# Optimization experiments

Hardware: AMD Instinct MI355X
Metric: run time of the kernel (lower is better)

The kernel has to match this reference:

```python
import jax, jax.numpy as jnp
import numpy as np

EPS = 1e-15
MAX_ATANH = 1.0 - 1e-5
V = 2097152   # total nodes (B*N*L flattened)
E = 8388608   # edges, ~avg degree 4 (temporal + parent/child)
ATT = 16
MAXD = 512    # mixer embedding table size
# curvature c = 1.0 (registered buffer, constant)


def _mobius_add(a, b):
    # Poincare ball Mobius addition, c = 1
    a2 = jnp.sum(a * a, -1, keepdims=True)
    b2 = jnp.sum(b * b, -1, keepdims=True)
    ab = jnp.sum(a * b, -1, keepdims=True)
    num = (1.0 + 2.0 * ab + b2) * a + (1.0 - a2) * b
    den = 1.0 + 2.0 * ab + a2 * b2
    return num / jnp.maximum(den, EPS)


def _log_map_x(x, y):
    # log_x(y): tangent vector at x pointing to y (c = 1)
    sub = _mobius_add(-x, y)
    n = jnp.maximum(jnp.linalg.norm(sub, axis=-1, keepdims=True), EPS)
    lam = 2.0 / jnp.maximum(1.0 - jnp.sum(x * x, -1, keepdims=True), EPS)
    return (2.0 / lam) * jnp.arctanh(jnp.minimum(n, MAX_ATANH)) * (sub / n)


def _exp_map_x(x, v):
    # exp_x(v) (c = 1)
    n = jnp.maximum(jnp.linalg.norm(v, axis=-1, keepdims=True), EPS)
    lam = 2.0 / jnp.maximum(1.0 - jnp.sum(x * x, -1, keepdims=True), EPS)
    return _mobius_add(x, jnp.tanh(0.5 * lam * n) * (v / n))


def setup_inputs() -> dict:
    key = jax.random.key(0)
    ks = jax.random.split(key, 8)
    # node embeddings strictly inside the unit ball: exp0 of a small tangent vec
    v0 = 0.5 * jax.random.normal(ks[0], (V, 2), jnp.float32)
    n0 = jnp.maximum(jnp.linalg.norm(v0, axis=-1, keepdims=True), EPS)
    x = jnp.tanh(n0) * v0 / n0
    edge_index = jax.random.randint(ks[1], (2, E), 0, V)
    depth = jax.random.randint(ks[2], (V,), 0, MAXD)
    W1 = jax.random.normal(ks[3], (2, ATT), jnp.float32) / jnp.sqrt(2.0)
    b1 = 0.1 * jax.random.normal(ks[4], (ATT,), jnp.float32)
    W2 = jax.random.normal(ks[5], (ATT, 1), jnp.float32) / jnp.sqrt(float(ATT))
    eta = jnp.float32(1.0)
    depth_scale = 1.0 + 0.01 * jax.random.normal(ks[6], (MAXD,), jnp.float32)
    depth_theta = 0.01 * jax.random.normal(ks[7], (MAXD,), jnp.float32)
    return {"x": x, "W1": W1, "b1": b1, "W2": W2, "eta": eta,
            "depth_scale": depth_scale, "depth_theta": depth_theta,
            "edge_index": edge_index, "depth": depth}


def reference(x, W1, b1, W2, eta, depth_scale, depth_theta, edge_index, depth):
    row, col = edge_index[0], edge_index[1]
    xi = x[row]                      # [E,2] gather target endpoints
    xj = x[col]                      # [E,2] gather source endpoints
    v_ij = _log_map_x(xi, xj)        # [E,2] hyperbolic log-map
    # small per-edge MLP scorer: Linear(2,16) -> GELU(exact) -> Linear(16,1)
    h = jax.nn.gelu(v_ij @ W1 + b1, approximate=False)
    scores = (h @ W2)[:, 0]          # [E]
    # segment softmax over target node (row)
    mx = jax.ops.segment_max(scores, row, num_segments=V)
    e = jnp.exp(scores - mx[row])
    den = jax.ops.segment_sum(e, row, num_segments=V)
    alpha = e / jnp.maximum(den[row], EPS)
    # scatter-add aggregate in tangent space
    m = jax.ops.segment_sum(alpha[:, None] * v_ij, row, num_segments=V)  # [V,2]
    # depth-gated mixer: per-node scale + 2D rotation
    d = jnp.minimum(depth, MAXD - 1)
    k = depth_scale[d][:, None]
    ang = depth_theta[d]
    ca, sa = jnp.cos(ang), jnp.sin(ang)
    m = k * jnp.stack([ca * m[:, 0] - sa * m[:, 1],
                       sa * m[:, 0] + ca * m[:, 1]], axis=-1)
    # exp-map update
    return _exp_map_x(x, eta * m)
```

## Files before the change

### kernel.cpp

```cpp
#include <hip/hip_runtime.h>
#include <math.h>

#define EPSF 1e-15f
#define MAX_ATANH (1.0f - 1e-5f)
#define ATT 16

#define LOG_NPB 10
#define NPB (1 << LOG_NPB)
#define MAXB 2048
#define NBLK 512

#define TDIM 512
#define TSPAN 12.5f
#define TSTEP (TSPAN / (float)(TDIM - 1))
#define TSCALE ((float)(TDIM - 1) / TSPAN)
#define TOFF (6.25f * TSCALE)

__device__ __forceinline__ float fast_atanh(float z) {
    return 0.5f * __logf(__fdividef(1.0f + z, 1.0f - z));
}

__device__ __forceinline__ float fast_tanh(float z) {
    return 1.0f - __fdividef(2.0f, __expf(2.0f * z) + 1.0f);
}

__device__ __forceinline__ float gelu_exact(float u) {
    return 0.5f * u * (1.0f + erff(u * 0.70710678118654752f));
}

__global__ void __launch_bounds__(256) build_table_kernel(
        const float* __restrict__ W1, const float* __restrict__ b1,
        const float* __restrict__ W2, float2* __restrict__ tab) {
    const int idx = blockIdx.x * 256 + threadIdx.x;
    if (idx >= TDIM * TDIM) return;
    const int iy = idx >> 9;
    const int ix = idx & (TDIM - 1);
    const float vy  = fmaf((float)iy, TSTEP, -6.25f);
    const float vx0 = fmaf((float)ix, TSTEP, -6.25f);
    const float vx1 = fmaf((float)min(ix + 1, TDIM - 1), TSTEP, -6.25f);
    float s0 = 0.0f, s1 = 0.0f;
    #pragma unroll
    for (int k = 0; k < ATT; ++k) {
        const float w1x = W1[k], w1y = W1[ATT + k], bb = b1[k], w2 = W2[k];
        const float u0 = fmaf(vx0, w1x, fmaf(vy, w1y, bb));
        const float u1 = fmaf(vx1, w1x, fmaf(vy, w1y, bb));
        s0 = fmaf(gelu_exact(u0), w2, s0);
        s1 = fmaf(gelu_exact(u1), w2, s1);
    }
    tab[idx] = make_float2(s0, s1);
}

__global__ void __launch_bounds__(256) hist_kernel(const int* __restrict__ row,
                                                   int E, int B,
                                                   unsigned* __restrict__ counts ) {
    __shared__ unsigned h[MAXB];
    for (int i = threadIdx.x; i < B; i += 256) h[i] = 0u;
    __syncthreads();
    const int T = gridDim.x * 256;
    const int nv = E >> 2;
    const int4* row4 = (const int4*)row;
    for (int i = blockIdx.x * 256 + threadIdx.x; i < nv; i += T) {
        const int4 r = row4[i];
        atomicAdd(&h[((unsigned)r.x) >> LOG_NPB], 1u);
        atomicAdd(&h[((unsigned)r.y) >> LOG_NPB], 1u);
        atomicAdd(&h[((unsigned)r.z) >> LOG_NPB], 1u);
        atomicAdd(&h[((unsigned)r.w) >> LOG_NPB], 1u);
    }
    for (int e = (nv << 2) + blockIdx.x * 256 + threadIdx.x; e < E; e += T)
        atomicAdd(&h[((unsigned)row[e]) >> LOG_NPB], 1u);
    __syncthreads();
    for (int i = threadIdx.x; i < B; i += 256)
        counts[(size_t)i * gridDim.x + blockIdx.x] = h[i];
}

__global__ void __launch_bounds__(256) scan_blocks_kernel(const unsigned* __restrict__ counts,
                                                          unsigned* __restrict__ within,
                                                          unsigned* __restrict__ totals) {
    const int b = blockIdx.x;
    const unsigned* src = counts + (size_t)b * NBLK;
    unsigned* dst = within + (size_t)b * NBLK;
    __shared__ unsigned s[256];
    unsigned v0, v1;
    {
        const uint2 v = ((const uint2*)src)[threadIdx.x];
        v0 = v.x; v1 = v.y;
    }
    s[threadIdx.x] = v0 + v1;
    __syncthreads();
    for (int off = 1; off < 256; off <<= 1) {
        unsigned t = (threadIdx.x >= off) ? s[threadIdx.x - off] : 0u;
        __syncthreads();
        s[threadIdx.x] += t;
        __syncthreads();
    }
    unsigned base = (threadIdx.x > 0) ? s[threadIdx.x - 1] : 0u;
    uint2 o;
    o.x = base; o.y = base + v0;
    ((uint2*)dst)[threadIdx.x] = o;
    if (threadIdx.x == 255) totals[b] = s[255];
}

__global__ void __launch_bounds__(256) scan_totals_kernel(const unsigned* __restrict__ totals,
                                                          unsigned* __restrict__ base, int B) {
    __shared__ unsigned s[256];
    unsigned vals[8];
    const int i0 = threadIdx.x * 8;
    unsigned sum = 0u;
    #pragma unroll
    for (int k = 0; k < 8; ++k) {
        vals[k] = (i0 + k < B) ? totals[i0 + k] : 0u;
        sum += vals[k];
    }
    s[threadIdx.x] = sum;
    __syncthreads();
    for (int off = 1; off < 256; off <<= 1) {
        unsigned t = (threadIdx.x >= off) ? s[threadIdx.x - off] : 0u;
        __syncthreads();
        s[threadIdx.x] += t;
        __syncthreads();
    }
    unsigned b0 = (threadIdx.x > 0) ? s[threadIdx.x - 1] : 0u;
    #pragma unroll
    for (int k = 0; k < 8; ++k) {
        if (i0 + k < B) base[i0 + k] = b0;
        b0 += vals[k];
    }
    if (threadIdx.x == 255) base[B] = s[255];
}

__global__ void __launch_bounds__(256) scatter_kernel(const int* __restrict__ row,
                                                      const int* __restrict__ col,
                                                      int E, int B,
                                                      const unsigned* __restrict__ base,
                                                      const unsigned* __restrict__ within,
                                                      unsigned* __restrict__ payload) {
    __shared__ unsigned cur[MAXB];
    const int nblk = gridDim.x;
    for (int i = threadIdx.x; i < B; i += 256)
        cur[i] = base[i] + within[(size_t)i * nblk + blockIdx.x];
    __syncthreads();
    const int T = nblk * 256;
    const int nv = E >> 2;
    const int4* row4 = (const int4*)row;
    const int4* col4 = (const int4*)col;
    for (int i = blockIdx.x * 256 + threadIdx.x; i < nv; i += T) {
        const int4 r = row4[i];
        const int4 c = col4[i];
        {
            const unsigned rr = (unsigned)r.x;
            const unsigned pos = atomicAdd(&cur[rr >> LOG_NPB], 1u);
            payload[pos] = ((rr & (NPB - 1)) << 21) | (unsigned)c.x;
        }
        {
            const unsigned rr = (unsigned)r.y;
            const unsigned pos = atomicAdd(&cur[rr >> LOG_NPB], 1u);
            payload[pos] = ((rr & (NPB - 1)) << 21) | (unsigned)c.y;
        }
        {
            const unsigned rr = (unsigned)r.z;
            const unsigned pos = atomicAdd(&cur[rr >> LOG_NPB], 1u);
            payload[pos] = ((rr & (NPB - 1)) << 21) | (unsigned)c.z;
        }
        {
            const unsigned rr = (unsigned)r.w;
            const unsigned pos = atomicAdd(&cur[rr >> LOG_NPB], 1u);
            payload[pos] = ((rr & (NPB - 1)) << 21) | (unsigned)c.w;
        }
    }
    for (int e = (nv << 2) + blockIdx.x * 256 + threadIdx.x; e < E; e += T) {
        const unsigned rr = (unsigned)row[e];
        const unsigned pos = atomicAdd(&cur[rr >> LOG_NPB], 1u);
        payload[pos] = ((rr & (NPB - 1)) << 21) | (unsigned)col[e];
    }
}

__global__ void __launch_bounds__(512, 8) bucket_reduce_kernel(
        const float2* __restrict__ x,
        const float2* __restrict__ tab,
        const unsigned* __restrict__ base,
        const unsigned* __restrict__ payload,
        const int* __restrict__ depth,
        const float* __restrict__ depth_scale,
        const float* __restrict__ depth_theta,
        const float* __restrict__ eta_p,
        float2* __restrict__ out, int V) {
    __shared__ float  sden[NPB];
    __shared__ float  smx[NPB];
    __shared__ float  smy[NPB];
    __shared__ float2 sxi[NPB];
    const int b = blockIdx.x;
    const int nodeBase = b << LOG_NPB;
    for (int i = threadIdx.x; i < NPB; i += 512) {
        sden[i] = 0.f; smx[i] = 0.f; smy[i] = 0.f;
        sxi[i] = x[nodeBase + i];
    }
    __syncthreads();

    const unsigned e0 = base[b], e1 = base[b + 1];
    for (unsigned e = e0 + threadIdx.x; e < e1; e += 512) {
        const unsigned p = payload[e];
        const unsigned lrow = p >> 21;
        const unsigned c = p & 0x1FFFFFu;
        const float2 xi = sxi[lrow];
        const float2 xj = x[c];

        const float ax = -xi.x, ay = -xi.y;
        const float bx = xj.x,  by = xj.y;
        const float a2 = ax * ax + ay * ay;
        const float b2 = bx * bx + by * by;
        const float ab = ax * bx + ay * by;
        const float ca = 1.0f + 2.0f * ab + b2;
        const float cb = 1.0f - a2;
        const float dn = fmaxf(1.0f + 2.0f * ab + a2 * b2, EPSF);
        const float rdn = __fdividef(1.0f, dn);
        const float subx = (ca * ax + cb * bx) * rdn;
        const float suby = (ca * ay + cb * by) * rdn;

        const float n = fmaxf(sqrtf(subx * subx + suby * suby), EPSF);
        const float M = fmaxf(1.0f - (xi.x * xi.x + xi.y * xi.y), EPSF);
        const float scl = M * fast_atanh(fminf(n, MAX_ATANH)) * __fdividef(1.0f, n);
        const float vx = scl * subx;
        const float vy = scl * suby;

        float tx = fmaf(vx, TSCALE, TOFF);
        float ty = fmaf(vy, TSCALE, TOFF);
        tx = fminf(fmaxf(tx, 0.0f), 510.999f);
        ty = fminf(fmaxf(ty, 0.0f), 510.999f);
        const int ix = (int)tx;
        const int iy = (int)ty;
        const float fx = tx - (float)ix;
        const float fy = ty - (float)iy;
        const int baseIdx = (iy << 9) + ix;
        const float2 r0 = tab[baseIdx];
        const float2 r1 = tab[baseIdx + TDIM];
        const float s0 = fmaf(fx, r0.y - r0.x, r0.x);
        const float s1 = fmaf(fx, r1.y - r1.x, r1.x);
        const float s  = fmaf(fy, s1 - s0, s0);

        const float ee = __expf(s);
        atomicAdd(&sden[lrow], ee);
        atomicAdd(&smx[lrow], ee * vx);
        atomicAdd(&smy[lrow], ee * vy);
    }
    __syncthreads();

    const float eta = eta_p[0];
    for (int i = threadIdx.x; i < NPB; i += 512) {
        const int v = nodeBase + i;
        if (v >= V) break;
        const float rdv = __fdividef(1.0f, fmaxf(sden[i], EPSF));
        const float mx = smx[i] * rdv;
        const float my = smy[i] * rdv;

        const int d = min(depth[v], 511);
        const float k   = depth_scale[d];
        const float ang = depth_theta[d];
        const float cs = __cosf(ang), sn = __sinf(ang);
        const float m0 = eta * (k * (cs * mx - sn * my));
        const float m1 = eta * (k * (sn * mx + cs * my));

        const float2 xi = sxi[i];

        const float n = fmaxf(sqrtf(m0 * m0 + m1 * m1), EPSF);
        const float M = fmaxf(1.0f - (xi.x * xi.x + xi.y * xi.y), EPSF);
        const float t = fast_tanh(__fdividef(n, M));
        const float tn = t * __fdividef(1.0f, n);
        const float bx = tn * m0;
        const float by = tn * m1;

        const float a2 = xi.x * xi.x + xi.y * xi.y;
        const float b2 = bx * bx + by * by;
        const float ab = xi.x * bx + xi.y * by;
        const float ca = 1.0f + 2.0f * ab + b2;
        const float cb = 1.0f - a2;
        const float dn = fmaxf(1.0f + 2.0f * ab + a2 * b2, EPSF);
        const float rdn = __fdividef(1.0f, dn);

        out[v] = make_float2((ca * xi.x + cb * bx) * rdn,
                             (ca * xi.y + cb * by) * rdn);
    }
}

extern "C" void kernel_launch(void* const* d_in, const int* in_sizes, int n_in,
                              void* d_out, int out_size, void* d_ws, size_t ws_size,
                              hipStream_t stream) {
    const float2* x          = (const float2*)d_in[0];
    const float*  W1         = (const float*)d_in[1];
    const float*  b1         = (const float*)d_in[2];
    const float*  W2         = (const float*)d_in[3];
    const float*  eta        = (const float*)d_in[4];
    const float*  dscale     = (const float*)d_in[5];
    const float*  dtheta     = (const float*)d_in[6];
    const int*    edge_index = (const int*)d_in[7];
    const int*    depth      = (const int*)d_in[8];

    const int V = in_sizes[0] / 2;
    const int E = in_sizes[7] / 2;
    const int B = (V + NPB - 1) >> LOG_NPB;

    const int* row = edge_index;
    const int* col = edge_index + E;

    unsigned* payload = (unsigned*)d_ws;
    unsigned* counts  = payload + E;
    unsigned* within  = counts + (size_t)B * NBLK;
    unsigned* totals  = within + (size_t)B * NBLK;
    unsigned* base    = totals + B;
    float2*   tab     = (float2*)within;

    hist_kernel<<<NBLK, 256, 0, stream>>>(row, E, B, counts);
    scan_blocks_kernel<<<B, 256, 0, stream>>>(counts, within, totals);
    scan_totals_kernel<<<1, 256, 0, stream>>>(totals, base, B);
    scatter_kernel<<<NBLK, 256, 0, stream>>>(row, col, E, B, base, within, payload);
    build_table_kernel<<<(TDIM * TDIM) / 256, 256, 0, stream>>>(W1, b1, W2, tab);
    bucket_reduce_kernel<<<B, 512, 0, stream>>>(x, tab, base, payload,
                                                depth, dscale, dtheta, eta,
                                                (float2*)d_out, V);
}
```

Measured before the change: 281.1 us.

## Scale histogram/scatter grid with workspace, add nontemporal loads and paired edge processing

Makes the histogram and scatter block count depend on available workspace (512, 1024 or 2048 blocks), with a templated block scan that handles the wider per-bucket count arrays. Streaming loads of row/col and payload become nontemporal, and the output store is nontemporal. The bucket reduce now reads payload in aligned pairs and peels the odd head and tail edges. More blocks add parallelism to the atomic-heavy sort phases but enlarge the counts/within arrays and the scan work; the table still aliases the within region, which needs enough space.

```diff
diff --git a/kernel.cpp b/kernel.cpp
--- a/kernel.cpp
+++ b/kernel.cpp
@@ -8,7 +8,6 @@
 #define LOG_NPB 10
 #define NPB (1 << LOG_NPB)
 #define MAXB 2048
-#define NBLK 512
 
 #define TDIM 512
 #define TSPAN 12.5f
@@ -16,14 +15,16 @@
 #define TSCALE ((float)(TDIM - 1) / TSPAN)
 #define TOFF (6.25f * TSCALE)
 
+typedef int    vint4  __attribute__((ext_vector_type(4)));
+typedef unsigned vuint2 __attribute__((ext_vector_type(2)));
+typedef float  vfloat2 __attribute__((ext_vector_type(2)));
+
 __device__ __forceinline__ float fast_atanh(float z) {
     return 0.5f * __logf(__fdividef(1.0f + z, 1.0f - z));
 }
-
 __device__ __forceinline__ float fast_tanh(float z) {
     return 1.0f - __fdividef(2.0f, __expf(2.0f * z) + 1.0f);
 }
-
 __device__ __forceinline__ float gelu_exact(float u) {
     return 0.5f * u * (1.0f + erff(u * 0.70710678118654752f));
 }
@@ -42,10 +43,8 @@
     #pragma unroll
     for (int k = 0; k < ATT; ++k) {
         const float w1x = W1[k], w1y = W1[ATT + k], bb = b1[k], w2 = W2[k];
-        const float u0 = fmaf(vx0, w1x, fmaf(vy, w1y, bb));
-        const float u1 = fmaf(vx1, w1x, fmaf(vy, w1y, bb));
-        s0 = fmaf(gelu_exact(u0), w2, s0);
-        s1 = fmaf(gelu_exact(u1), w2, s1);
+        s0 = fmaf(gelu_exact(fmaf(vx0, w1x, fmaf(vy, w1y, bb))), w2, s0);
+        s1 = fmaf(gelu_exact(fmaf(vx1, w1x, fmaf(vy, w1y, bb))), w2, s1);
     }
     tab[idx] = make_float2(s0, s1);
 }
@@ -58,9 +57,9 @@
     __syncthreads();
     const int T = gridDim.x * 256;
     const int nv = E >> 2;
-    const int4* row4 = (const int4*)row;
+    const vint4* row4 = (const vint4*)row;
     for (int i = blockIdx.x * 256 + threadIdx.x; i < nv; i += T) {
-        const int4 r = row4[i];
+        const vint4 r = __builtin_nontemporal_load(&row4[i]);
         atomicAdd(&h[((unsigned)r.x) >> LOG_NPB], 1u);
         atomicAdd(&h[((unsigned)r.y) >> LOG_NPB], 1u);
         atomicAdd(&h[((unsigned)r.z) >> LOG_NPB], 1u);
@@ -73,19 +72,32 @@
         counts[(size_t)i * gridDim.x + blockIdx.x] = h[i];
 }
 
+template<int K>
 __global__ void __launch_bounds__(256) scan_blocks_kernel(const unsigned* __restrict__ counts,
                                                           unsigned* __restrict__ within,
-                                                          unsigned* __restrict__ totals) {
+                                                          unsigned* __restrict__ totals,
+                                                          int nblk) {
     const int b = blockIdx.x;
-    const unsigned* src = counts + (size_t)b * NBLK;
-    unsigned* dst = within + (size_t)b * NBLK;
+    const unsigned* src = counts + (size_t)b * nblk;
+    unsigned* dst = within + (size_t)b * nblk;
     __shared__ unsigned s[256];
-    unsigned v0, v1;
-    {
+    unsigned vals[K];
+    unsigned sum = 0u;
+    if constexpr (K == 2) {
         const uint2 v = ((const uint2*)src)[threadIdx.x];
-        v0 = v.x; v1 = v.y;
-    }
-    s[threadIdx.x] = v0 + v1;
+        vals[0] = v.x; vals[1] = v.y;
+    } else if constexpr (K == 4) {
+        const uint4 v = ((const uint4*)src)[threadIdx.x];
+        vals[0] = v.x; vals[1] = v.y; vals[2] = v.z; vals[3] = v.w;
+    } else {
+        const uint4 va = ((const uint4*)src)[threadIdx.x * 2];
+        const uint4 vb = ((const uint4*)src)[threadIdx.x * 2 + 1];
+        vals[0] = va.x; vals[1] = va.y; vals[2] = va.z; vals[3] = va.w;
+        vals[4] = vb.x; vals[5] = vb.y; vals[6] = vb.z; vals[7] = vb.w;
+    }
+    #pragma unroll
+    for (int k = 0; k < K; ++k) sum += vals[k];
+    s[threadIdx.x] = sum;
     __syncthreads();
     for (int off = 1; off < 256; off <<= 1) {
         unsigned t = (threadIdx.x >= off) ? s[threadIdx.x - off] : 0u;
@@ -93,10 +105,23 @@
         s[threadIdx.x] += t;
         __syncthreads();
     }
-    unsigned base = (threadIdx.x > 0) ? s[threadIdx.x - 1] : 0u;
-    uint2 o;
-    o.x = base; o.y = base + v0;
-    ((uint2*)dst)[threadIdx.x] = o;
+    unsigned run = (threadIdx.x > 0) ? s[threadIdx.x - 1] : 0u;
+    unsigned outv[K];
+    #pragma unroll
+    for (int k = 0; k < K; ++k) { outv[k] = run; run += vals[k]; }
+    if constexpr (K == 2) {
+        uint2 o; o.x = outv[0]; o.y = outv[1];
+        ((uint2*)dst)[threadIdx.x] = o;
+    } else if constexpr (K == 4) {
+        uint4 o; o.x = outv[0]; o.y = outv[1]; o.z = outv[2]; o.w = outv[3];
+        ((uint4*)dst)[threadIdx.x] = o;
+    } else {
+        uint4 oa, ob;
+        oa.x = outv[0]; oa.y = outv[1]; oa.z = outv[2]; oa.w = outv[3];
+        ob.x = outv[4]; ob.y = outv[5]; ob.z = outv[6]; ob.w = outv[7];
+        ((uint4*)dst)[threadIdx.x * 2]     = oa;
+        ((uint4*)dst)[threadIdx.x * 2 + 1] = ob;
+    }
     if (threadIdx.x == 255) totals[b] = s[255];
 }
 
@@ -141,11 +166,11 @@
     __syncthreads();
     const int T = nblk * 256;
     const int nv = E >> 2;
-    const int4* row4 = (const int4*)row;
-    const int4* col4 = (const int4*)col;
+    const vint4* row4 = (const vint4*)row;
+    const vint4* col4 = (const vint4*)col;
     for (int i = blockIdx.x * 256 + threadIdx.x; i < nv; i += T) {
-        const int4 r = row4[i];
-        const int4 c = col4[i];
+        const vint4 r = __builtin_nontemporal_load(&row4[i]);
+        const vint4 c = __builtin_nontemporal_load(&col4[i]);
         {
             const unsigned rr = (unsigned)r.x;
             const unsigned pos = atomicAdd(&cur[rr >> LOG_NPB], 1u);
@@ -174,6 +199,53 @@
     }
 }
 
+__device__ __forceinline__ void edge_math(unsigned p,
+        const float2* __restrict__ x, const float2* __restrict__ tab,
+        const float2* sxi, float* sden, float* smx, float* smy) {
+    const unsigned lrow = p >> 21;
+    const unsigned c = p & 0x1FFFFFu;
+    const float2 xj = x[c];
+    const float2 xi = sxi[lrow];
+
+    const float ax = -xi.x, ay = -xi.y;
+    const float bx = xj.x,  by = xj.y;
+    const float a2 = ax * ax + ay * ay;
+    const float b2 = bx * bx + by * by;
+    const float ab = ax * bx + ay * by;
+    const float ca = 1.0f + 2.0f * ab + b2;
+    const float cb = 1.0f - a2;
+    const float dn = fmaxf(1.0f + 2.0f * ab + a2 * b2, EPSF);
+    const float rdn = __fdividef(1.0f, dn);
+    const float subx = (ca * ax + cb * bx) * rdn;
+    const float suby = (ca * ay + cb * by) * rdn;
+
+    const float n = fmaxf(sqrtf(subx * subx + suby * suby), EPSF);
+    const float M = fmaxf(1.0f - (xi.x * xi.x + xi.y * xi.y), EPSF);
+    const float scl = M * fast_atanh(fminf(n, MAX_ATANH)) * __fdividef(1.0f, n);
+    const float vx = scl * subx;
+    const float vy = scl * suby;
+
+    float tx = fmaf(vx, TSCALE, TOFF);
+    float ty = fmaf(vy, TSCALE, TOFF);
+    tx = fminf(fmaxf(tx, 0.0f), 510.999f);
+    ty = fminf(fmaxf(ty, 0.0f), 510.999f);
+    const int ix = (int)tx;
+    const int iy = (int)ty;
+    const float fx = tx - (float)ix;
+    const float fy = ty - (float)iy;
+    const int baseIdx = (iy << 9) + ix;
+    const float2 r0 = tab[baseIdx];
+    const float2 r1 = tab[baseIdx + TDIM];
+    const float s0 = fmaf(fx, r0.y - r0.x, r0.x);
+    const float s1 = fmaf(fx, r1.y - r1.x, r1.x);
+    const float s  = fmaf(fy, s1 - s0, s0);
+
+    const float ee = __expf(s);
+    atomicAdd(&sden[lrow], ee);
+    atomicAdd(&smx[lrow], ee * vx);
+    atomicAdd(&smy[lrow], ee * vy);
+}
+
 __global__ void __launch_bounds__(512, 8) bucket_reduce_kernel(
         const float2* __restrict__ x,
         const float2* __restrict__ tab,
@@ -197,51 +269,22 @@
     __syncthreads();
 
     const unsigned e0 = base[b], e1 = base[b + 1];
-    for (unsigned e = e0 + threadIdx.x; e < e1; e += 512) {
-        const unsigned p = payload[e];
-        const unsigned lrow = p >> 21;
-        const unsigned c = p & 0x1FFFFFu;
-        const float2 xi = sxi[lrow];
-        const float2 xj = x[c];
-
-        const float ax = -xi.x, ay = -xi.y;
-        const float bx = xj.x,  by = xj.y;
-        const float a2 = ax * ax + ay * ay;
-        const float b2 = bx * bx + by * by;
-        const float ab = ax * bx + ay * by;
-        const float ca = 1.0f + 2.0f * ab + b2;
-        const float cb = 1.0f - a2;
-        const float dn = fmaxf(1.0f + 2.0f * ab + a2 * b2, EPSF);
-        const float rdn = __fdividef(1.0f, dn);
-        const float subx = (ca * ax + cb * bx) * rdn;
-        const float suby = (ca * ay + cb * by) * rdn;
-
-        const float n = fmaxf(sqrtf(subx * subx + suby * suby), EPSF);
-        const float M = fmaxf(1.0f - (xi.x * xi.x + xi.y * xi.y), EPSF);
-        const float scl = M * fast_atanh(fminf(n, MAX_ATANH)) * __fdividef(1.0f, n);
-        const float vx = scl * subx;
-        const float vy = scl * suby;
-
-        float tx = fmaf(vx, TSCALE, TOFF);
-        float ty = fmaf(vy, TSCALE, TOFF);
-        tx = fminf(fmaxf(tx, 0.0f), 510.999f);
-        ty = fminf(fmaxf(ty, 0.0f), 510.999f);
-        const int ix = (int)tx;
-        const int iy = (int)ty;
-        const float fx = tx - (float)ix;
-        const float fy = ty - (float)iy;
-        const int baseIdx = (iy << 9) + ix;
-        const float2 r0 = tab[baseIdx];
-        const float2 r1 = tab[baseIdx + TDIM];
-        const float s0 = fmaf(fx, r0.y - r0.x, r0.x);
-        const float s1 = fmaf(fx, r1.y - r1.x, r1.x);
-        const float s  = fmaf(fy, s1 - s0, s0);
-
-        const float ee = __expf(s);
-        atomicAdd(&sden[lrow], ee);
-        atomicAdd(&smx[lrow], ee * vx);
-        atomicAdd(&smy[lrow], ee * vy);
-    }
+    unsigned s0 = e0;
+    if ((s0 & 1u) && s0 < e1) {
+        if (threadIdx.x == 0)
+            edge_math(payload[s0], x, tab, sxi, sden, smx, smy);
+        ++s0;
+    }
+    const unsigned cnt = (e1 > s0) ? (e1 - s0) : 0u;
+    const unsigned pairs = cnt >> 1;
+    const vuint2* pay2 = (const vuint2*)(payload + s0);
+    for (unsigned k = threadIdx.x; k < pairs; k += 512) {
+        const vuint2 pp = __builtin_nontemporal_load(&pay2[k]);
+        edge_math(pp.x, x, tab, sxi, sden, smx, smy);
+        edge_math(pp.y, x, tab, sxi, sden, smx, smy);
+    }
+    if ((cnt & 1u) && threadIdx.x == 0)
+        edge_math(payload[s0 + (pairs << 1)], x, tab, sxi, sden, smx, smy);
     __syncthreads();
 
     const float eta = eta_p[0];
@@ -276,8 +319,10 @@
         const float dn = fmaxf(1.0f + 2.0f * ab + a2 * b2, EPSF);
         const float rdn = __fdividef(1.0f, dn);
 
-        out[v] = make_float2((ca * xi.x + cb * bx) * rdn,
-                             (ca * xi.y + cb * by) * rdn);
+        vfloat2 o;
+        o.x = (ca * xi.x + cb * bx) * rdn;
+        o.y = (ca * xi.y + cb * by) * rdn;
+        __builtin_nontemporal_store(o, (vfloat2*)&out[v]);
     }
 }
 
@@ -301,17 +346,29 @@
     const int* row = edge_index;
     const int* col = edge_index + E;
 
+    auto need = [&](int nblk) -> size_t {
+        return ((size_t)E + 2 * (size_t)B * nblk + 2 * (size_t)B + 2) * 4;
+    };
+    int nblk = 512;
+    if (ws_size >= need(2048)) nblk = 2048;
+    else if (ws_size >= need(1024)) nblk = 1024;
+
     unsigned* payload = (unsigned*)d_ws;
     unsigned* counts  = payload + E;
-    unsigned* within  = counts + (size_t)B * NBLK;
-    unsigned* totals  = within + (size_t)B * NBLK;
+    unsigned* within  = counts + (size_t)B * nblk;
+    unsigned* totals  = within + (size_t)B * nblk;
     unsigned* base    = totals + B;
     float2*   tab     = (float2*)within;
 
-    hist_kernel<<<NBLK, 256, 0, stream>>>(row, E, B, counts);
-    scan_blocks_kernel<<<B, 256, 0, stream>>>(counts, within, totals);
+    hist_kernel<<<nblk, 256, 0, stream>>>(row, E, B, counts);
+    if (nblk == 2048)
+        scan_blocks_kernel<8><<<B, 256, 0, stream>>>(counts, within, totals, nblk);
+    else if (nblk == 1024)
+        scan_blocks_kernel<4><<<B, 256, 0, stream>>>(counts, within, totals, nblk);
+    else
+        scan_blocks_kernel<2><<<B, 256, 0, stream>>>(counts, within, totals, nblk);
     scan_totals_kernel<<<1, 256, 0, stream>>>(totals, base, B);
-    scatter_kernel<<<NBLK, 256, 0, stream>>>(row, col, E, B, base, within, payload);
+    scatter_kernel<<<nblk, 256, 0, stream>>>(row, col, E, B, base, within, payload);
     build_table_kernel<<<(TDIM * TDIM) / 256, 256, 0, stream>>>(W1, b1, W2, tab);
     bucket_reduce_kernel<<<B, 512, 0, stream>>>(x, tab, base, payload,
                                                 depth, dscale, dtheta, eta,
```

After: 358.5 us. +27.5%, slower.
